# Optimization experiments

Hardware: AMD Instinct MI355X
Metric: run time of the kernel (lower is better)

Reference implementation:

```python
import jax, jax.numpy as jnp
import numpy as np

B, N, M, C, H = 4, 2048, 2048, 1024, 16
D = C // H  # head_dim = 64
SCALE = D ** -0.5


def setup_inputs() -> dict:
    key = jax.random.key(0)
    ks = jax.random.split(key, 8)
    std = C ** -0.5
    return {
        "query": jax.random.normal(ks[0], (B, N, C), jnp.float32),
        "key": jax.random.normal(ks[1], (B, M, C), jnp.float32),
        "value": jax.random.normal(ks[2], (B, M, C), jnp.float32),
        "Wq": jax.random.normal(ks[3], (C, C), jnp.float32) * std,
        "Wk": jax.random.normal(ks[4], (C, C), jnp.float32) * std,
        "Wv": jax.random.normal(ks[5], (C, C), jnp.float32) * std,
        "Wp": jax.random.normal(ks[6], (C, C), jnp.float32) * std,
        "bp": jax.random.normal(ks[7], (C,), jnp.float32) * 0.01,
    }


def reference(query, key, value, Wq, Wk, Wv, Wp, bp):
    # Linear: y = x @ W.T (torch nn.Linear convention), no bias for q/k/v.
    # reshape (B,S,C)->(B,S,H,D)->(B,H,S,D)
    q = jnp.einsum('bnc,dc->bnd', query, Wq).reshape(B, N, H, D).transpose(0, 2, 1, 3)
    k = jnp.einsum('bmc,dc->bmd', key, Wk).reshape(B, M, H, D).transpose(0, 2, 1, 3)
    v = jnp.einsum('bmc,dc->bmd', value, Wv).reshape(B, M, H, D).transpose(0, 2, 1, 3)
    # scaled scores, softmax over keys
    attn = jnp.einsum('bhnd,bhmd->bhnm', q * SCALE, k)
    attn = jax.nn.softmax(attn, axis=-1)
    # attention output -> (B,N,C)
    x = jnp.einsum('bhnm,bhmd->bhnd', attn, v).transpose(0, 2, 1, 3).reshape(B, N, C)
    # output projection with bias
    return jnp.einsum('bnc,dc->bnd', x, Wp) + bp
```

## Files before the change

kernel.cpp:

```cpp
#include <hip/hip_runtime.h>
#include <stdint.h>

#define B_ 4
#define N_ 2048
#define M_ 2048
#define C_ 1024
#define H_ 16
#define D_ 64
#define SC_ (B_*N_*C_)
#define CC_ (C_*C_)

typedef unsigned short u16;
typedef __attribute__((ext_vector_type(8))) short short8;
typedef __attribute__((ext_vector_type(4))) short short4v;
typedef __attribute__((ext_vector_type(4))) float f32x4;

#if __has_builtin(__builtin_amdgcn_exp2f)
#define EXP2F __builtin_amdgcn_exp2f
#else
#define EXP2F exp2f
#endif

__device__ inline u16 f2bf(float f) {
    union { float f; uint32_t u; } v; v.f = f;
    uint32_t r = v.u + 0x7fffu + ((v.u >> 16) & 1u);
    return (u16)(r >> 16);
}

__device__ inline f32x4 mfma16x16x16_bf16(short4v a, short4v b, f32x4 c) {
#if __has_builtin(__builtin_amdgcn_mfma_f32_16x16x16bf16_1k)
    return __builtin_amdgcn_mfma_f32_16x16x16bf16_1k(a, b, c, 0, 0, 0);
#else
    asm volatile("v_mfma_f32_16x16x16_bf16 %0, %1, %2, %0"
                 : "+v"(c) : "v"(a), "v"(b));
    return c;
#endif
}

#define WAIT_BARRIER(N)                                         \
    do {                                                        \
        asm volatile("s_waitcnt vmcnt(" #N ")" ::: "memory");   \
        __builtin_amdgcn_s_barrier();                           \
        __builtin_amdgcn_sched_barrier(0);                      \
    } while (0)

__global__ __launch_bounds__(256) void convert_kernel(
    const float* __restrict__ q, const float* __restrict__ k, const float* __restrict__ v,
    const float* __restrict__ wq, const float* __restrict__ wk,
    const float* __restrict__ wv, const float* __restrict__ wp,
    u16* __restrict__ qf, u16* __restrict__ kf, u16* __restrict__ vf,
    u16* __restrict__ wqb, u16* __restrict__ wkb, u16* __restrict__ wvb, u16* __restrict__ wpb)
{
    const int SC4 = SC_ / 4;
    const int CC4 = CC_ / 4;
    const int total = 3 * SC4 + 4 * CC4;
    for (int i = blockIdx.x * 256 + threadIdx.x; i < total; i += gridDim.x * 256) {
        const float* src; u16* dst; int off;
        if (i < 3 * SC4) {
            int seg = i >> 21;
            off = (i & (SC4 - 1)) << 2;
            src = seg == 0 ? q : seg == 1 ? k : v;
            dst = seg == 0 ? qf : seg == 1 ? kf : vf;
        } else {
            int j = i - 3 * SC4;
            int seg = j >> 18;
            off = (j & (CC4 - 1)) << 2;
            src = seg == 0 ? wq : seg == 1 ? wk : seg == 2 ? wv : wp;
            dst = seg == 0 ? wqb : seg == 1 ? wkb : seg == 2 ? wvb : wpb;
        }
        float4 val = *(const float4*)(src + off);
        ushort4 h;
        h.x = f2bf(val.x); h.y = f2bf(val.y); h.z = f2bf(val.z); h.w = f2bf(val.w);
        *(ushort4*)(dst + off) = h;
    }
}

__global__ __launch_bounds__(256, 3) void gemm_qkv(
    const u16* __restrict__ A0, const u16* __restrict__ W0, u16* __restrict__ O0,
    const u16* __restrict__ A1, const u16* __restrict__ W1, u16* __restrict__ O1,
    const u16* __restrict__ A2, const u16* __restrict__ W2, u16* __restrict__ O2,
    float qscale)
{
    const int K = 1024;
    __shared__ u16 SH[3 * 8192];
    const int tid = threadIdx.x;
    const int wid = tid >> 6, lane = tid & 63;
    const int quad = lane >> 4, l15 = lane & 15;
    const int gseg = blockIdx.x >> 9;
    const int f = blockIdx.x & 511;
    const u16* A  = gseg == 0 ? A0 : gseg == 1 ? A1 : A2;
    const u16* Wb = gseg == 0 ? W0 : gseg == 1 ? W1 : W2;
    u16* Op       = gseg == 0 ? O0 : gseg == 1 ? O1 : O2;
    const float scale = gseg == 2 ? qscale : 1.0f;

    const int m0 = (f & 63) * 128, n0 = (f >> 6) * 128;
    const int wm = (wid >> 1) * 64, wn = (wid & 1) * 64;

    size_t aoff[2], boff[2];
    int dsto[2];
#pragma unroll
    for (int i = 0; i < 2; ++i) {
        int s = tid + i * 256;
        int row = s >> 2, c8 = (s & 3) << 3;
        aoff[i] = (size_t)(m0 + row) * K + c8;
        boff[i] = (size_t)(n0 + row) * K + c8;
        dsto[i] = s * 8;
    }

    f32x4 acc[4][4];
#pragma unroll
    for (int i = 0; i < 4; ++i)
#pragma unroll
        for (int j = 0; j < 4; ++j) acc[i][j] = f32x4{0.f, 0.f, 0.f, 0.f};

#pragma unroll
    for (int t = 0; t < 2; ++t) {
        const int bo = t * 8192, k0 = t * 32;
#pragma unroll
        for (int i = 0; i < 2; ++i) {
            __builtin_amdgcn_global_load_lds(
                (const __attribute__((address_space(1))) void*)(A + aoff[i] + k0),
                (__attribute__((address_space(3))) void*)(SH + bo + dsto[i]), 16, 0, 0);
            __builtin_amdgcn_global_load_lds(
                (const __attribute__((address_space(1))) void*)(Wb + boff[i] + k0),
                (__attribute__((address_space(3))) void*)(SH + bo + 4096 + dsto[i]), 16, 0, 0);
        }
    }

    for (int it = 0; it < 32; ++it) {
        const int cur = (it % 3) * 8192;
        if (it < 31) WAIT_BARRIER(4);
        else         WAIT_BARRIER(0);
        if (it + 2 < 32) {
            const int nxt = ((it + 2) % 3) * 8192;
            const int k0n = (it + 2) * 32;
#pragma unroll
            for (int i = 0; i < 2; ++i) {
                __builtin_amdgcn_global_load_lds(
                    (const __attribute__((address_space(1))) void*)(A + aoff[i] + k0n),
                    (__attribute__((address_space(3))) void*)(SH + nxt + dsto[i]), 16, 0, 0);
                __builtin_amdgcn_global_load_lds(
                    (const __attribute__((address_space(1))) void*)(Wb + boff[i] + k0n),
                    (__attribute__((address_space(3))) void*)(SH + nxt + 4096 + dsto[i]), 16, 0, 0);
            }
        }
        short8 av[4], bv[4];
#pragma unroll
        for (int i = 0; i < 4; ++i)
            av[i] = *(const short8*)(SH + cur + (wm + i * 16 + l15) * 32 + quad * 8);
#pragma unroll
        for (int j = 0; j < 4; ++j)
            bv[j] = *(const short8*)(SH + cur + 4096 + (wn + j * 16 + l15) * 32 + quad * 8);
#pragma unroll
        for (int i = 0; i < 4; ++i)
#pragma unroll
            for (int j = 0; j < 4; ++j)
                acc[i][j] = __builtin_amdgcn_mfma_f32_16x16x32_bf16(av[i], bv[j], acc[i][j], 0, 0, 0);
    }

    if (gseg == 1) {
#pragma unroll
        for (int j = 0; j < 4; ++j) {
            int col = n0 + wn + j * 16 + l15;
            int hh = col >> 6, dd = col & 63;
#pragma unroll
            for (int i = 0; i < 4; ++i) {
                int row = m0 + wm + i * 16 + quad * 4;
                int bb = row >> 11, mm = row & 2047;
                ushort4 hv;
                hv.x = f2bf(acc[i][j][0]);
                hv.y = f2bf(acc[i][j][1]);
                hv.z = f2bf(acc[i][j][2]);
                hv.w = f2bf(acc[i][j][3]);
                *(ushort4*)(Op + (((size_t)bb * 16 + hh) * 64 + dd) * 2048 + mm) = hv;
            }
        }
    } else {
#pragma unroll
        for (int j = 0; j < 4; ++j) {
            int col = n0 + wn + j * 16 + l15;
#pragma unroll
            for (int i = 0; i < 4; ++i) {
                int row = m0 + wm + i * 16 + quad * 4;
#pragma unroll
                for (int r = 0; r < 4; ++r)
                    Op[(size_t)(row + r) * 1024 + col] = f2bf(acc[i][j][r] * scale);
            }
        }
    }
}

__global__ __launch_bounds__(256) void gemm_p(
    const u16* __restrict__ A, const u16* __restrict__ Wb,
    const float* __restrict__ bias, float* __restrict__ Op)
{
    const int K = 1024;
    __shared__ u16 SH[3 * 8192];
    const int tid = threadIdx.x;
    const int wid = tid >> 6, lane = tid & 63;
    const int quad = lane >> 4, l15 = lane & 15;
    const int f = blockIdx.x;
    const int m0 = (f & 63) * 128, n0 = (f >> 6) * 128;
    const int wm = (wid >> 1) * 64, wn = (wid & 1) * 64;

    size_t aoff[2], boff[2];
    int dsto[2];
#pragma unroll
    for (int i = 0; i < 2; ++i) {
        int s = tid + i * 256;
        int row = s >> 2, c8 = (s & 3) << 3;
        aoff[i] = (size_t)(m0 + row) * K + c8;
        boff[i] = (size_t)(n0 + row) * K + c8;
        dsto[i] = s * 8;
    }

    f32x4 acc[4][4];
#pragma unroll
    for (int i = 0; i < 4; ++i)
#pragma unroll
        for (int j = 0; j < 4; ++j) acc[i][j] = f32x4{0.f, 0.f, 0.f, 0.f};

#pragma unroll
    for (int t = 0; t < 2; ++t) {
        const int bo = t * 8192, k0 = t * 32;
#pragma unroll
        for (int i = 0; i < 2; ++i) {
            __builtin_amdgcn_global_load_lds(
                (const __attribute__((address_space(1))) void*)(A + aoff[i] + k0),
                (__attribute__((address_space(3))) void*)(SH + bo + dsto[i]), 16, 0, 0);
            __builtin_amdgcn_global_load_lds(
                (const __attribute__((address_space(1))) void*)(Wb + boff[i] + k0),
                (__attribute__((address_space(3))) void*)(SH + bo + 4096 + dsto[i]), 16, 0, 0);
        }
    }

    for (int it = 0; it < 32; ++it) {
        const int cur = (it % 3) * 8192;
        if (it < 31) WAIT_BARRIER(4);
        else         WAIT_BARRIER(0);
        if (it + 2 < 32) {
            const int nxt = ((it + 2) % 3) * 8192;
            const int k0n = (it + 2) * 32;
#pragma unroll
            for (int i = 0; i < 2; ++i) {
                __builtin_amdgcn_global_load_lds(
                    (const __attribute__((address_space(1))) void*)(A + aoff[i] + k0n),
                    (__attribute__((address_space(3))) void*)(SH + nxt + dsto[i]), 16, 0, 0);
                __builtin_amdgcn_global_load_lds(
                    (const __attribute__((address_space(1))) void*)(Wb + boff[i] + k0n),
                    (__attribute__((address_space(3))) void*)(SH + nxt + 4096 + dsto[i]), 16, 0, 0);
            }
        }
        short8 av[4], bv[4];
#pragma unroll
        for (int i = 0; i < 4; ++i)
            av[i] = *(const short8*)(SH + cur + (wm + i * 16 + l15) * 32 + quad * 8);
#pragma unroll
        for (int j = 0; j < 4; ++j)
            bv[j] = *(const short8*)(SH + cur + 4096 + (wn + j * 16 + l15) * 32 + quad * 8);
#pragma unroll
        for (int i = 0; i < 4; ++i)
#pragma unroll
            for (int j = 0; j < 4; ++j)
                acc[i][j] = __builtin_amdgcn_mfma_f32_16x16x32_bf16(av[i], bv[j], acc[i][j], 0, 0, 0);
    }

#pragma unroll
    for (int j = 0; j < 4; ++j) {
        int col = n0 + wn + j * 16 + l15;
        float bb = bias[col];
#pragma unroll
        for (int i = 0; i < 4; ++i) {
            int row = m0 + wm + i * 16 + quad * 4;
#pragma unroll
            for (int r = 0; r < 4; ++r)
                Op[(size_t)(row + r) * 1024 + col] = acc[i][j][r] + bb;
        }
    }
}

__global__ __launch_bounds__(256, 3) void attn_kernel(
    const u16* __restrict__ qg, const u16* __restrict__ kg,
    const u16* __restrict__ vT, u16* __restrict__ xb)
{
    __shared__ __align__(16) u16 KV[2 * 8192];

    const int tid = threadIdx.x;
    const int wid = tid >> 6, lane = tid & 63;
    const int quad = lane >> 4, l15 = lane & 15;
    const int f = blockIdx.x;
    const int bh = f & 63, qt = f >> 6;
    const int b = bh >> 4, h = bh & 15;

    const u16* qbase = qg + ((size_t)(b * N_ + qt * 128 + wid * 32)) * C_ + h * 64;
    short8 qf[2][2];
#pragma unroll
    for (int qb2 = 0; qb2 < 2; ++qb2)
#pragma unroll
        for (int ch = 0; ch < 2; ++ch)
            qf[qb2][ch] = *(const short8*)(qbase + (size_t)(qb2 * 16 + l15) * C_ + ch * 32 + quad * 8);

    const u16* kptr[2];
    const u16* vptr[2];
    int dsto[2];
#pragma unroll
    for (int i = 0; i < 2; ++i) {
        int s = tid + i * 256;
        int row = s >> 3, g = s & 7;
        int gsw = g ^ (row & 7);
        kptr[i] = kg + ((size_t)(b * M_ + row)) * C_ + h * 64 + gsw * 8;
        vptr[i] = vT + (((size_t)b * 16 + h) * 64 + row) * M_ + gsw * 8;
        dsto[i] = s * 8;
    }

    f32x4 acc[4][2];
#pragma unroll
    for (int i = 0; i < 4; ++i)
#pragma unroll
        for (int j = 0; j < 2; ++j) acc[i][j] = f32x4{0.f, 0.f, 0.f, 0.f};
    float lsum[2] = {0.f, 0.f};

    const int swr = l15 & 7;
    const int kxo0 = ((0 * 4 + quad) ^ swr) << 3;
    const int kxo1 = ((1 * 4 + quad) ^ swr) << 3;
    int vbase[4];
#pragma unroll
    for (int db = 0; db < 4; ++db)
        vbase[db] = 4096 + (db * 16 + l15) * 64 + ((quad & 1) << 2);
    int vx[4];
#pragma unroll
    for (int kt = 0; kt < 4; ++kt)
        vx[kt] = ((kt * 2 + (quad >> 1)) ^ swr) << 3;

    union { short4v s; uint32_t u[2]; } pfrag[2], vfu;

#pragma unroll
    for (int i = 0; i < 2; ++i) {
        __builtin_amdgcn_global_load_lds(
            (const __attribute__((address_space(1))) void*)(kptr[i]),
            (__attribute__((address_space(3))) void*)(KV + dsto[i]), 16, 0, 0);
        __builtin_amdgcn_global_load_lds(
            (const __attribute__((address_space(1))) void*)(vptr[i]),
            (__attribute__((address_space(3))) void*)(KV + 4096 + dsto[i]), 16, 0, 0);
    }

    for (int it = 0; it < 32; ++it) {
        const int cur = (it & 1) * 8192;
        __syncthreads();
        if (it + 1 < 32) {
            const int nxt = ((it + 1) & 1) * 8192;
            const int kvn = (it + 1) * 64;
#pragma unroll
            for (int i = 0; i < 2; ++i) {
                __builtin_amdgcn_global_load_lds(
                    (const __attribute__((address_space(1))) void*)(kptr[i] + (size_t)kvn * C_),
                    (__attribute__((address_space(3))) void*)(KV + nxt + dsto[i]), 16, 0, 0);
                __builtin_amdgcn_global_load_lds(
                    (const __attribute__((address_space(1))) void*)(vptr[i] + kvn),
                    (__attribute__((address_space(3))) void*)(KV + nxt + 4096 + dsto[i]), 16, 0, 0);
            }
        }

#pragma unroll
        for (int kt = 0; kt < 4; ++kt) {
            const int kbase = cur + (kt * 16 + l15) * 64;
            short8 kf0 = *(const short8*)(KV + kbase + kxo0);
            short8 kf1 = *(const short8*)(KV + kbase + kxo1);
            f32x4 sc0 = f32x4{0.f, 0.f, 0.f, 0.f};
            f32x4 sc1 = f32x4{0.f, 0.f, 0.f, 0.f};
            sc0 = __builtin_amdgcn_mfma_f32_16x16x32_bf16(kf0, qf[0][0], sc0, 0, 0, 0);
            sc1 = __builtin_amdgcn_mfma_f32_16x16x32_bf16(kf0, qf[1][0], sc1, 0, 0, 0);
            sc0 = __builtin_amdgcn_mfma_f32_16x16x32_bf16(kf1, qf[0][1], sc0, 0, 0, 0);
            sc1 = __builtin_amdgcn_mfma_f32_16x16x32_bf16(kf1, qf[1][1], sc1, 0, 0, 0);

#pragma unroll
            for (int qb2 = 0; qb2 < 2; ++qb2) {
                const f32x4 sv = qb2 ? sc1 : sc0;
                float e0 = EXP2F(sv[0]);
                float e1 = EXP2F(sv[1]);
                float e2 = EXP2F(sv[2]);
                float e3 = EXP2F(sv[3]);
                lsum[qb2] += (e0 + e1) + (e2 + e3);
                pfrag[qb2].u[0] = __builtin_amdgcn_perm(__builtin_bit_cast(uint32_t, e1),
                                                        __builtin_bit_cast(uint32_t, e0), 0x07060302u);
                pfrag[qb2].u[1] = __builtin_amdgcn_perm(__builtin_bit_cast(uint32_t, e3),
                                                        __builtin_bit_cast(uint32_t, e2), 0x07060302u);
            }

#pragma unroll
            for (int db = 0; db < 4; ++db) {
                uint2 vlo = *(const uint2*)(KV + cur + vbase[db] + vx[kt]);
                vfu.u[0] = vlo.x; vfu.u[1] = vlo.y;
                acc[db][0] = mfma16x16x16_bf16(vfu.s, pfrag[0].s, acc[db][0]);
                acc[db][1] = mfma16x16x16_bf16(vfu.s, pfrag[1].s, acc[db][1]);
            }
        }
    }

    lsum[0] += __shfl_xor(lsum[0], 16);
    lsum[0] += __shfl_xor(lsum[0], 32);
    lsum[1] += __shfl_xor(lsum[1], 16);
    lsum[1] += __shfl_xor(lsum[1], 32);
    const float dinv[2] = {1.f / lsum[0], 1.f / lsum[1]};

#pragma unroll
    for (int qb2 = 0; qb2 < 2; ++qb2) {
        size_t ob = ((size_t)(b * N_ + qt * 128 + wid * 32 + qb2 * 16 + l15)) * C_ + h * 64;
#pragma unroll
        for (int db = 0; db < 4; ++db) {
            ushort4 st;
            st.x = f2bf(acc[db][qb2][0] * dinv[qb2]);
            st.y = f2bf(acc[db][qb2][1] * dinv[qb2]);
            st.z = f2bf(acc[db][qb2][2] * dinv[qb2]);
            st.w = f2bf(acc[db][qb2][3] * dinv[qb2]);
            *(ushort4*)(xb + ob + db * 16 + quad * 4) = st;
        }
    }
}

extern "C" void kernel_launch(void* const* d_in, const int* in_sizes, int n_in,
                              void* d_out, int out_size, void* d_ws, size_t ws_size,
                              hipStream_t stream) {
    const float* query = (const float*)d_in[0];
    const float* key   = (const float*)d_in[1];
    const float* value = (const float*)d_in[2];
    const float* Wq    = (const float*)d_in[3];
    const float* Wk    = (const float*)d_in[4];
    const float* Wv    = (const float*)d_in[5];
    const float* Wpm   = (const float*)d_in[6];
    const float* bp    = (const float*)d_in[7];
    float* out = (float*)d_out;

    u16* base = (u16*)d_ws;
    u16* qf  = base;
    u16* kf  = base + (size_t)SC_;
    u16* vf  = base + (size_t)2 * SC_;
    u16* kb  = base + (size_t)3 * SC_;
    u16* Wqb = base + (size_t)4 * SC_;
    u16* Wkb = Wqb + CC_;
    u16* Wvb = Wkb + CC_;
    u16* Wpb = Wvb + CC_;
    u16* vTp = kf;
    u16* qb  = vf;
    u16* xb  = qf;

    hipLaunchKernelGGL(convert_kernel, dim3(4096), dim3(256), 0, stream,
                       query, key, value, Wq, Wk, Wv, Wpm,
                       qf, kf, vf, Wqb, Wkb, Wvb, Wpb);

    hipLaunchKernelGGL(gemm_qkv, dim3(1536), dim3(256), 0, stream,
                       kf, Wkb, kb,
                       vf, Wvb, Wpb + CC_,
                       qf, Wqb, qb,
                       0.125f * 1.44269504088896340736f);

    u16* vTr = Wpb + CC_;

    hipLaunchKernelGGL(attn_kernel, dim3(1024), dim3(256), 0, stream, qb, kb, vTr, xb);

    hipLaunchKernelGGL(gemm_p, dim3(512), dim3(256), 0, stream, xb, Wpb, bp, out);
}
```

Baseline: 330.7 us.

## Stage V tiles through registers into padded LDS rows in attention kernel

The attention kernel stops loading V tiles with direct global-to-LDS copies into XOR-swizzled rows. It now prefetches V two iterations ahead into registers and writes it to LDS rows padded to 72 elements, so the PV MFMA operand becomes one contiguous short4 read with simpler addressing and fewer bank conflicts. The loop is manually unrolled by two to ping-pong the register buffers. The GEMM global-to-LDS calls are wrapped in a helper, which is cosmetic. The change costs more VGPRs and LDS, which could lower occupancy under launch_bounds(256,3).

```diff
diff --git a/kernel.cpp b/kernel.cpp
--- a/kernel.cpp
+++ b/kernel.cpp
@@ -35,6 +35,12 @@
                  : "+v"(c) : "v"(a), "v"(b));
     return c;
 #endif
+}
+
+__device__ inline void gll16(const u16* g, u16* l) {
+    __builtin_amdgcn_global_load_lds(
+        (const __attribute__((address_space(1))) void*)g,
+        (__attribute__((address_space(3))) void*)l, 16, 0, 0);
 }
 
 #define WAIT_BARRIER(N)                                         \
@@ -118,12 +124,8 @@
         const int bo = t * 8192, k0 = t * 32;
 #pragma unroll
         for (int i = 0; i < 2; ++i) {
-            __builtin_amdgcn_global_load_lds(
-                (const __attribute__((address_space(1))) void*)(A + aoff[i] + k0),
-                (__attribute__((address_space(3))) void*)(SH + bo + dsto[i]), 16, 0, 0);
-            __builtin_amdgcn_global_load_lds(
-                (const __attribute__((address_space(1))) void*)(Wb + boff[i] + k0),
-                (__attribute__((address_space(3))) void*)(SH + bo + 4096 + dsto[i]), 16, 0, 0);
+            gll16(A + aoff[i] + k0, SH + bo + dsto[i]);
+            gll16(Wb + boff[i] + k0, SH + bo + 4096 + dsto[i]);
         }
     }
 
@@ -136,12 +138,8 @@
             const int k0n = (it + 2) * 32;
 #pragma unroll
             for (int i = 0; i < 2; ++i) {
-                __builtin_amdgcn_global_load_lds(
-                    (const __attribute__((address_space(1))) void*)(A + aoff[i] + k0n),
-                    (__attribute__((address_space(3))) void*)(SH + nxt + dsto[i]), 16, 0, 0);
-                __builtin_amdgcn_global_load_lds(
-                    (const __attribute__((address_space(1))) void*)(Wb + boff[i] + k0n),
-                    (__attribute__((address_space(3))) void*)(SH + nxt + 4096 + dsto[i]), 16, 0, 0);
+                gll16(A + aoff[i] + k0n, SH + nxt + dsto[i]);
+                gll16(Wb + boff[i] + k0n, SH + nxt + 4096 + dsto[i]);
             }
         }
         short8 av[4], bv[4];
@@ -225,12 +223,8 @@
         const int bo = t * 8192, k0 = t * 32;
 #pragma unroll
         for (int i = 0; i < 2; ++i) {
-            __builtin_amdgcn_global_load_lds(
-                (const __attribute__((address_space(1))) void*)(A + aoff[i] + k0),
-                (__attribute__((address_space(3))) void*)(SH + bo + dsto[i]), 16, 0, 0);
-            __builtin_amdgcn_global_load_lds(
-                (const __attribute__((address_space(1))) void*)(Wb + boff[i] + k0),
-                (__attribute__((address_space(3))) void*)(SH + bo + 4096 + dsto[i]), 16, 0, 0);
+            gll16(A + aoff[i] + k0, SH + bo + dsto[i]);
+            gll16(Wb + boff[i] + k0, SH + bo + 4096 + dsto[i]);
         }
     }
 
@@ -243,12 +237,8 @@
             const int k0n = (it + 2) * 32;
 #pragma unroll
             for (int i = 0; i < 2; ++i) {
-                __builtin_amdgcn_global_load_lds(
-                    (const __attribute__((address_space(1))) void*)(A + aoff[i] + k0n),
-                    (__attribute__((address_space(3))) void*)(SH + nxt + dsto[i]), 16, 0, 0);
-                __builtin_amdgcn_global_load_lds(
-                    (const __attribute__((address_space(1))) void*)(Wb + boff[i] + k0n),
-                    (__attribute__((address_space(3))) void*)(SH + nxt + 4096 + dsto[i]), 16, 0, 0);
+                gll16(A + aoff[i] + k0n, SH + nxt + dsto[i]);
+                gll16(Wb + boff[i] + k0n, SH + nxt + 4096 + dsto[i]);
             }
         }
         short8 av[4], bv[4];
@@ -283,7 +273,7 @@
     const u16* __restrict__ qg, const u16* __restrict__ kg,
     const u16* __restrict__ vT, u16* __restrict__ xb)
 {
-    __shared__ __align__(16) u16 KV[2 * 8192];
+    __shared__ __align__(16) u16 KV[2 * 8704];
 
     const int tid = threadIdx.x;
     const int wid = tid >> 6, lane = tid & 63;
@@ -301,16 +291,24 @@
             qf[qb2][ch] = *(const short8*)(qbase + (size_t)(qb2 * 16 + l15) * C_ + ch * 32 + quad * 8);
 
     const u16* kptr[2];
-    const u16* vptr[2];
-    int dsto[2];
+    int kdst[2];
 #pragma unroll
     for (int i = 0; i < 2; ++i) {
         int s = tid + i * 256;
         int row = s >> 3, g = s & 7;
         int gsw = g ^ (row & 7);
         kptr[i] = kg + ((size_t)(b * M_ + row)) * C_ + h * 64 + gsw * 8;
-        vptr[i] = vT + (((size_t)b * 16 + h) * 64 + row) * M_ + gsw * 8;
-        dsto[i] = s * 8;
+        kdst[i] = s * 8;
+    }
+
+    const u16* vsrc[2];
+    int vdst[2];
+#pragma unroll
+    for (int i = 0; i < 2; ++i) {
+        int idx = tid + i * 256;
+        int vrow = idx >> 3, c8 = idx & 7;
+        vsrc[i] = vT + (((size_t)b * 16 + h) * 64 + vrow) * M_ + c8 * 8;
+        vdst[i] = 4096 + vrow * 72 + c8 * 8;
     }
 
     f32x4 acc[4][2];
@@ -323,79 +321,78 @@
     const int swr = l15 & 7;
     const int kxo0 = ((0 * 4 + quad) ^ swr) << 3;
     const int kxo1 = ((1 * 4 + quad) ^ swr) << 3;
-    int vbase[4];
+    int voff[4];
 #pragma unroll
     for (int db = 0; db < 4; ++db)
-        vbase[db] = 4096 + (db * 16 + l15) * 64 + ((quad & 1) << 2);
-    int vx[4];
-#pragma unroll
-    for (int kt = 0; kt < 4; ++kt)
-        vx[kt] = ((kt * 2 + (quad >> 1)) ^ swr) << 3;
-
-    union { short4v s; uint32_t u[2]; } pfrag[2], vfu;
-
-#pragma unroll
-    for (int i = 0; i < 2; ++i) {
-        __builtin_amdgcn_global_load_lds(
-            (const __attribute__((address_space(1))) void*)(kptr[i]),
-            (__attribute__((address_space(3))) void*)(KV + dsto[i]), 16, 0, 0);
-        __builtin_amdgcn_global_load_lds(
-            (const __attribute__((address_space(1))) void*)(vptr[i]),
-            (__attribute__((address_space(3))) void*)(KV + 4096 + dsto[i]), 16, 0, 0);
-    }
-
-    for (int it = 0; it < 32; ++it) {
-        const int cur = (it & 1) * 8192;
-        __syncthreads();
-        if (it + 1 < 32) {
-            const int nxt = ((it + 1) & 1) * 8192;
-            const int kvn = (it + 1) * 64;
-#pragma unroll
-            for (int i = 0; i < 2; ++i) {
-                __builtin_amdgcn_global_load_lds(
-                    (const __attribute__((address_space(1))) void*)(kptr[i] + (size_t)kvn * C_),
-                    (__attribute__((address_space(3))) void*)(KV + nxt + dsto[i]), 16, 0, 0);
-                __builtin_amdgcn_global_load_lds(
-                    (const __attribute__((address_space(1))) void*)(vptr[i] + kvn),
-                    (__attribute__((address_space(3))) void*)(KV + nxt + 4096 + dsto[i]), 16, 0, 0);
-            }
-        }
-
-#pragma unroll
-        for (int kt = 0; kt < 4; ++kt) {
-            const int kbase = cur + (kt * 16 + l15) * 64;
-            short8 kf0 = *(const short8*)(KV + kbase + kxo0);
-            short8 kf1 = *(const short8*)(KV + kbase + kxo1);
-            f32x4 sc0 = f32x4{0.f, 0.f, 0.f, 0.f};
-            f32x4 sc1 = f32x4{0.f, 0.f, 0.f, 0.f};
-            sc0 = __builtin_amdgcn_mfma_f32_16x16x32_bf16(kf0, qf[0][0], sc0, 0, 0, 0);
-            sc1 = __builtin_amdgcn_mfma_f32_16x16x32_bf16(kf0, qf[1][0], sc1, 0, 0, 0);
-            sc0 = __builtin_amdgcn_mfma_f32_16x16x32_bf16(kf1, qf[0][1], sc0, 0, 0, 0);
-            sc1 = __builtin_amdgcn_mfma_f32_16x16x32_bf16(kf1, qf[1][1], sc1, 0, 0, 0);
-
-#pragma unroll
-            for (int qb2 = 0; qb2 < 2; ++qb2) {
-                const f32x4 sv = qb2 ? sc1 : sc0;
-                float e0 = EXP2F(sv[0]);
-                float e1 = EXP2F(sv[1]);
-                float e2 = EXP2F(sv[2]);
-                float e3 = EXP2F(sv[3]);
-                lsum[qb2] += (e0 + e1) + (e2 + e3);
-                pfrag[qb2].u[0] = __builtin_amdgcn_perm(__builtin_bit_cast(uint32_t, e1),
-                                                        __builtin_bit_cast(uint32_t, e0), 0x07060302u);
-                pfrag[qb2].u[1] = __builtin_amdgcn_perm(__builtin_bit_cast(uint32_t, e3),
-                                                        __builtin_bit_cast(uint32_t, e2), 0x07060302u);
-            }
-
-#pragma unroll
-            for (int db = 0; db < 4; ++db) {
-                uint2 vlo = *(const uint2*)(KV + cur + vbase[db] + vx[kt]);
-                vfu.u[0] = vlo.x; vfu.u[1] = vlo.y;
-                acc[db][0] = mfma16x16x16_bf16(vfu.s, pfrag[0].s, acc[db][0]);
-                acc[db][1] = mfma16x16x16_bf16(vfu.s, pfrag[1].s, acc[db][1]);
-            }
-        }
-    }
+        voff[db] = 4096 + (db * 16 + l15) * 72 + quad * 4;
+
+    union { short4v s; uint32_t u[2]; } pfrag[2];
+
+    short8 vstA[2], vstB[2];
+
+    gll16(kptr[0], KV + kdst[0]);
+    gll16(kptr[1], KV + kdst[1]);
+    vstA[0] = *(const short8*)(vsrc[0]);
+    vstA[1] = *(const short8*)(vsrc[1]);
+    vstB[0] = *(const short8*)(vsrc[0] + 64);
+    vstB[1] = *(const short8*)(vsrc[1] + 64);
+    *(short8*)(KV + vdst[0]) = vstA[0];
+    *(short8*)(KV + vdst[1]) = vstA[1];
+
+#define ATTN_BODY(IT, VW, VL)                                                  \
+    {                                                                          \
+        const int cur = ((IT) & 1) * 8704;                                     \
+        const int nxtb = (((IT) + 1) & 1) * 8704;                              \
+        __syncthreads();                                                       \
+        if ((IT) + 1 < 32) {                                                   \
+            *(short8*)(KV + nxtb + vdst[0]) = VW[0];                           \
+            *(short8*)(KV + nxtb + vdst[1]) = VW[1];                           \
+            const size_t kvn = (size_t)((IT) + 1) * 64;                        \
+            gll16(kptr[0] + kvn * C_, KV + nxtb + kdst[0]);                    \
+            gll16(kptr[1] + kvn * C_, KV + nxtb + kdst[1]);                    \
+        }                                                                      \
+        if ((IT) + 2 < 32) {                                                   \
+            VL[0] = *(const short8*)(vsrc[0] + ((IT) + 2) * 64);               \
+            VL[1] = *(const short8*)(vsrc[1] + ((IT) + 2) * 64);               \
+        }                                                                      \
+        _Pragma("unroll")                                                      \
+        for (int kt = 0; kt < 4; ++kt) {                                       \
+            const int kbase = cur + (kt * 16 + l15) * 64;                      \
+            short8 kf0 = *(const short8*)(KV + kbase + kxo0);                  \
+            short8 kf1 = *(const short8*)(KV + kbase + kxo1);                  \
+            f32x4 sc0 = f32x4{0.f, 0.f, 0.f, 0.f};                             \
+            f32x4 sc1 = f32x4{0.f, 0.f, 0.f, 0.f};                             \
+            sc0 = __builtin_amdgcn_mfma_f32_16x16x32_bf16(kf0, qf[0][0], sc0, 0, 0, 0); \
+            sc1 = __builtin_amdgcn_mfma_f32_16x16x32_bf16(kf0, qf[1][0], sc1, 0, 0, 0); \
+            sc0 = __builtin_amdgcn_mfma_f32_16x16x32_bf16(kf1, qf[0][1], sc0, 0, 0, 0); \
+            sc1 = __builtin_amdgcn_mfma_f32_16x16x32_bf16(kf1, qf[1][1], sc1, 0, 0, 0); \
+            _Pragma("unroll")                                                  \
+            for (int qb2 = 0; qb2 < 2; ++qb2) {                                \
+                const f32x4 sv = qb2 ? sc1 : sc0;                              \
+                float e0 = EXP2F(sv[0]);                                       \
+                float e1 = EXP2F(sv[1]);                                       \
+                float e2 = EXP2F(sv[2]);                                       \
+                float e3 = EXP2F(sv[3]);                                       \
+                lsum[qb2] += (e0 + e1) + (e2 + e3);                            \
+                pfrag[qb2].u[0] = __builtin_amdgcn_perm(__builtin_bit_cast(uint32_t, e1), \
+                                                        __builtin_bit_cast(uint32_t, e0), 0x07060302u); \
+                pfrag[qb2].u[1] = __builtin_amdgcn_perm(__builtin_bit_cast(uint32_t, e3), \
+                                                        __builtin_bit_cast(uint32_t, e2), 0x07060302u); \
+            }                                                                  \
+            _Pragma("unroll")                                                  \
+            for (int db = 0; db < 4; ++db) {                                   \
+                short4v vv = *(const short4v*)(KV + cur + voff[db] + kt * 16); \
+                acc[db][0] = mfma16x16x16_bf16(vv, pfrag[0].s, acc[db][0]);    \
+                acc[db][1] = mfma16x16x16_bf16(vv, pfrag[1].s, acc[db][1]);    \
+            }                                                                  \
+        }                                                                      \
+    }
+
+    for (int it2 = 0; it2 < 16; ++it2) {
+        ATTN_BODY(2 * it2,     vstB, vstA);
+        ATTN_BODY(2 * it2 + 1, vstA, vstB);
+    }
+#undef ATTN_BODY
 
     lsum[0] += __shfl_xor(lsum[0], 16);
     lsum[0] += __shfl_xor(lsum[0], 32);
@@ -440,9 +437,9 @@
     u16* Wkb = Wqb + CC_;
     u16* Wvb = Wkb + CC_;
     u16* Wpb = Wvb + CC_;
-    u16* vTp = kf;
     u16* qb  = vf;
     u16* xb  = qf;
+    u16* vTr = Wpb + CC_;
 
     hipLaunchKernelGGL(convert_kernel, dim3(4096), dim3(256), 0, stream,
                        query, key, value, Wq, Wk, Wv, Wpm,
@@ -450,12 +447,10 @@
 
     hipLaunchKernelGGL(gemm_qkv, dim3(1536), dim3(256), 0, stream,
                        kf, Wkb, kb,
-                       vf, Wvb, Wpb + CC_,
+                       vf, Wvb, vTr,
                        qf, Wqb, qb,
                        0.125f * 1.44269504088896340736f);
 
-    u16* vTr = Wpb + CC_;
-
     hipLaunchKernelGGL(attn_kernel, dim3(1024), dim3(256), 0, stream, qb, kb, vTr, xb);
 
     hipLaunchKernelGGL(gemm_p, dim3(512), dim3(256), 0, stream, xb, Wpb, bp, out);
```

Result: no change. 334.3 us (+1.1%).
